# Performance work log

Measured on AMD Instinct MI355X. Metric: run time of the kernel, lower is better.

The kernel has to match this reference:

```python
import jax, jax.numpy as jnp
from jax import lax
import numpy as np


def _qlayer(x, theta):
    """Simulate QLayer: RX(x_i) encoder + trainable RX(theta_i) per wire
    (they commute -> single RX(x_i+theta_i) on |0>), then ring of CNOTs,
    then <Z> on each wire.  x: (B, n) float, theta: (n,). Returns (B, n)."""
    B, n = x.shape
    a = x + theta[None, :]
    c = jnp.cos(a * 0.5)
    s = jnp.sin(a * 0.5)
    # RX(a)|0> = [cos(a/2), -i sin(a/2)] per wire -> product state
    amps = jnp.stack([c + 0j, -1j * s], axis=-1)  # (B, n, 2) complex64
    state = amps[:, 0]  # (B, 2)
    for w in range(1, n):
        state = state[..., None] * amps[:, w].reshape((B,) + (1,) * w + (2,))
    # state: (B, 2, 2, ..., 2), axis w+1 == wire w
    for ctrl in range(n):
        tgt = (ctrl + 1) % n
        s0 = jnp.take(state, 0, axis=ctrl + 1)   # control = 0 block
        s1 = jnp.take(state, 1, axis=ctrl + 1)   # control = 1 block
        t_ax = tgt + 1 if tgt < ctrl else tgt    # target axis after removing ctrl axis
        s1 = jnp.flip(s1, axis=t_ax)             # X on target
        state = jnp.stack([s0, s1], axis=ctrl + 1)
    p = state.real ** 2 + state.imag ** 2
    axes = tuple(range(1, n + 1))
    zs = []
    for w in range(n):
        other = tuple(ax for ax in axes if ax != w + 1)
        pw = jnp.sum(p, axis=other)              # (B, 2)
        zs.append(pw[:, 0] - pw[:, 1])           # <Z_w> = P(0) - P(1)
    return jnp.stack(zs, axis=1)


def setup_inputs() -> dict:
    key = jax.random.key(0)
    ks = jax.random.split(key, 13)
    T, B, D, NQ = 64, 256, 512, 6
    lim = 1.0 / np.sqrt(D + NQ)

    def lin(k):
        k1, k2 = jax.random.split(k)
        W = jax.random.uniform(k1, (D + NQ, NQ), jnp.float32, -lim, lim)
        b = jax.random.uniform(k2, (NQ,), jnp.float32, -lim, lim)
        return W, b

    Wf, bf = lin(ks[0]); Wi, bi = lin(ks[1]); Wu, bu = lin(ks[2]); Wo, bo = lin(ks[3])
    theta_f = jax.random.normal(ks[4], (NQ,), jnp.float32) * 0.1
    theta_i = jax.random.normal(ks[5], (NQ,), jnp.float32) * 0.1
    theta_u = jax.random.normal(ks[6], (NQ,), jnp.float32) * 0.1
    theta_o = jax.random.normal(ks[7], (NQ,), jnp.float32) * 0.1
    inputs = jax.random.normal(ks[8], (T, B, D), jnp.float32)
    return {"inputs": inputs,
            "Wf": Wf, "bf": bf, "Wi": Wi, "bi": bi,
            "Wu": Wu, "bu": bu, "Wo": Wo, "bo": bo,
            "theta_f": theta_f, "theta_i": theta_i,
            "theta_u": theta_u, "theta_o": theta_o}


def reference(inputs, Wf, bf, Wi, bi, Wu, bu, Wo, bo,
              theta_f, theta_i, theta_u, theta_o):
    B = inputs.shape[1]
    NQ = theta_f.shape[0]  # hidden_dim == n_qubits
    h0 = jnp.zeros((B, NQ), inputs.dtype)
    c0 = jnp.zeros((B, NQ), inputs.dtype)

    def step(carry, x):
        hx, cx = carry
        comb = jnp.concatenate([x, hx], axis=1)          # (B, D+NQ)
        f = jax.nn.sigmoid(_qlayer(comb @ Wf + bf, theta_f))
        i = jax.nn.sigmoid(_qlayer(comb @ Wi + bi, theta_i))
        g = jnp.tanh(_qlayer(comb @ Wu + bu, theta_u))
        o = jax.nn.sigmoid(_qlayer(comb @ Wo + bo, theta_o))
        cx2 = f * cx + i * g
        hx2 = o * jnp.tanh(cx2)
        return (hx2, cx2), hx2

    (hx, cx), outputs = lax.scan(step, (h0, c0), inputs)  # outputs: (T, B, NQ)
    return outputs, hx, cx
```

## Files before the change

kernel.cpp:

```cpp
#include <hip/hip_runtime.h>


typedef float v2f __attribute__((ext_vector_type(2)));

__device__ __forceinline__ float fast_rcp(float x) { return __builtin_amdgcn_rcpf(x); }

template <int CTRL>
__device__ __forceinline__ float dpp_add(float x) {
    int t = __builtin_amdgcn_mov_dpp(__float_as_int(x), CTRL, 0xF, 0xF, true);
    return x + __int_as_float(t);
}

template <int G>
__device__ __forceinline__ float quad_bcast(float v) {
    int i = __builtin_amdgcn_mov_dpp(__float_as_int(v), G * 0x55, 0xF, 0xF, true);
    return __int_as_float(i);
}

__global__ __launch_bounds__(512, 2) void gemm_pre(
    const float* __restrict__ X,
    const float* __restrict__ Wf, const float* __restrict__ bf,
    const float* __restrict__ Wi, const float* __restrict__ bi,
    const float* __restrict__ Wu, const float* __restrict__ bu,
    const float* __restrict__ Wo, const float* __restrict__ bo,
    const float* __restrict__ thf, const float* __restrict__ thi,
    const float* __restrict__ thu, const float* __restrict__ tho,
    float* __restrict__ pre)
{
    __shared__ float W_lds[13312];

    const int tid  = threadIdx.x;
    const int w    = tid >> 6;
    const int lane = tid & 63;
    const int rowbase = blockIdx.x * 32;

    #pragma unroll
    for (int i = 0; i < 4; ++i) {
        const float* Wp = (i==0)?Wf:(i==1)?Wi:(i==2)?Wu:Wo;
        int k = tid;
        const float2* s = (const float2*)(Wp + k*6);
        float2* d = (float2*)(W_lds + k*26 + i*6);
        d[0] = s[0]; d[1] = s[1]; d[2] = s[2];
    }
    __syncthreads();

    v2f acc[4][12];
    #pragma unroll
    for (int r = 0; r < 4; ++r)
        #pragma unroll
        for (int p = 0; p < 12; ++p) acc[r][p] = (v2f){0.f, 0.f};

    const float* Xr0 = X + (rowbase + w*4)*512 + lane;

    float pa0 = Xr0[0], pa1 = Xr0[512], pa2 = Xr0[1024], pa3 = Xr0[1536];
    #pragma unroll
    for (int kb = 0; kb < 512; kb += 64) {
        float a0 = pa0, a1 = pa1, a2 = pa2, a3 = pa3;
        if (kb < 448) {
            pa0 = Xr0[kb + 64];
            pa1 = Xr0[kb + 64 + 512];
            pa2 = Xr0[kb + 64 + 1024];
            pa3 = Xr0[kb + 64 + 1536];
        }
        const v2f* wrow = (const v2f*)(W_lds + (kb + lane)*26);
        #pragma unroll
        for (int p = 0; p < 12; ++p) {
            v2f wv = wrow[p];
            acc[0][p] = __builtin_elementwise_fma((v2f){a0,a0}, wv, acc[0][p]);
            acc[1][p] = __builtin_elementwise_fma((v2f){a1,a1}, wv, acc[1][p]);
            acc[2][p] = __builtin_elementwise_fma((v2f){a2,a2}, wv, acc[2][p]);
            acc[3][p] = __builtin_elementwise_fma((v2f){a3,a3}, wv, acc[3][p]);
        }
    }

    #pragma unroll
    for (int r = 0; r < 4; ++r)
        #pragma unroll
        for (int p = 0; p < 12; ++p) {
            float x = acc[r][p].x;
            x = dpp_add<0xB1>(x);
            x = dpp_add<0x4E>(x);
            acc[r][p].x = x;
            float y = acc[r][p].y;
            y = dpp_add<0xB1>(y);
            y = dpp_add<0x4E>(y);
            acc[r][p].y = y;
        }

    #define ACCV(v) ((((v) & 1) == 0) ? acc[(v)/24][((v)%24)/2].x \
                                      : acc[(v)/24][((v)%24)/2].y)
    const int j = lane & 3;
    const int q = lane >> 2;
    const bool j1 = (j & 1) != 0, j2 = (j & 2) != 0;
    float sel[24];
    #pragma unroll
    for (int i = 0; i < 24; ++i) {
        float c0 = ACCV(i*4 + 0), c1 = ACCV(i*4 + 1);
        float c2 = ACCV(i*4 + 2), c3 = ACCV(i*4 + 3);
        float lo = j1 ? c1 : c0;
        float hi = j1 ? c3 : c2;
        sel[i] = j2 ? hi : lo;
    }
    #undef ACCV

    __syncthreads();
    #pragma unroll
    for (int i = 0; i < 24; ++i) {
        W_lds[(w*96 + i*4 + j)*16 + q] = sel[i];
    }
    __syncthreads();

    for (int o = tid; o < 768; o += 512) {
        int ww = o / 96, v = o - ww*96;
        int rr = v / 24, jj24 = v - rr*24;
        const float4* rp = (const float4*)(W_lds + (ww*96 + v)*16);
        float4 r0 = rp[0], r1 = rp[1], r2 = rp[2], r3 = rp[3];
        float s = ((r0.x+r0.y)+(r0.z+r0.w)) + ((r1.x+r1.y)+(r1.z+r1.w))
                + ((r2.x+r2.y)+(r2.z+r2.w)) + ((r3.x+r3.y)+(r3.z+r3.w));
        int g = jj24 / 6, jg = jj24 - g*6;
        const float* bb = (g==0)?bf:(g==1)?bi:(g==2)?bu:bo;
        const float* tt = (g==0)?thf:(g==1)?thi:(g==2)?thu:tho;
        s += bb[jg] + tt[jg];
        int row = rowbase + ww*4 + rr;
        pre[row*24 + jj24] = s;
    }
}

__global__ __launch_bounds__(64, 1) void qlstm_scan(
    const float* __restrict__ pre,
    const float* __restrict__ Wf, const float* __restrict__ Wi,
    const float* __restrict__ Wu, const float* __restrict__ Wo,
    float* __restrict__ out)
{
    const int lane = threadIdx.x;
    const int bl   = lane >> 2;
    const int g    = lane & 3;
    const int b    = blockIdx.x * 16 + bl;

    const float* Wg = (g==0)?Wf:(g==1)?Wi:(g==2)?Wu:Wo;
    float Wh[6][6];
    #pragma unroll
    for (int j = 0; j < 6; ++j)
        #pragma unroll
        for (int w = 0; w < 6; ++w)
            Wh[j][w] = Wg[(512 + j)*6 + w];

    const float k1 = (g==2) ? 2.f : 1.f;
    const float k2 = (g==2) ? 2.f : 1.f;
    const float k3 = (g==2) ? -1.f : 0.f;

    float h[6], c[6];
    #pragma unroll
    for (int w = 0; w < 6; ++w) { h[w] = 0.f; c[w] = 0.f; }

    const float* pb = pre + b*24 + g*6;
    float2 x0 = *(const float2*)(pb);
    float2 x1 = *(const float2*)(pb + 2);
    float2 x2 = *(const float2*)(pb + 4);
    float2 n0 = *(const float2*)(pb + 256*24);
    float2 n1 = *(const float2*)(pb + 256*24 + 2);
    float2 n2 = *(const float2*)(pb + 256*24 + 4);

    for (int t = 0; t < 64; ++t) {
        float xw[6] = {x0.x, x0.y, x1.x, x1.y, x2.x, x2.y};
        x0 = n0; x1 = n1; x2 = n2;
        int tn = (t < 62) ? (t + 2) : 63;
        const float* pn = pre + (tn*256 + b)*24 + g*6;
        n0 = *(const float2*)(pn);
        n1 = *(const float2*)(pn + 2);
        n2 = *(const float2*)(pn + 4);

        float a[6];
        #pragma unroll
        for (int w = 0; w < 6; ++w) {
            float cA = fmaf(h[2], Wh[2][w], fmaf(h[1], Wh[1][w], fmaf(h[0], Wh[0][w], xw[w])));
            float cB = fmaf(h[5], Wh[5][w], fmaf(h[4], Wh[4][w], h[3]*Wh[3][w]));
            a[w] = cA + cB;
        }

        float C[6];
        #pragma unroll
        for (int w = 0; w < 6; ++w) C[w] = __cosf(a[w]);

        float p01 = C[0]*C[1], p23 = C[2]*C[3], p45 = C[4]*C[5];
        float z[6];
        z[1] = p01;
        z[2] = p01*C[2];
        z[3] = p01*p23;
        z[4] = z[3]*C[4];
        z[5] = z[3]*p45;
        z[0] = C[1]*(p23*p45);

        float act[6];
        #pragma unroll
        for (int w = 0; w < 6; ++w) {
            float e = __expf(-k1 * z[w]);
            act[w] = fmaf(k2, fast_rcp(1.f + e), k3);
        }

        float F[6], I[6], U[6], O[6];
        #pragma unroll
        for (int w = 0; w < 6; ++w) {
            F[w] = quad_bcast<0>(act[w]);
            I[w] = quad_bcast<1>(act[w]);
            U[w] = quad_bcast<2>(act[w]);
            O[w] = quad_bcast<3>(act[w]);
        }

        #pragma unroll
        for (int w = 0; w < 6; ++w) {
            c[w] = fmaf(F[w], c[w], I[w]*U[w]);
            float e  = __expf(-2.f * c[w]);
            float tc = fmaf(2.f, fast_rcp(1.f + e), -1.f);
            h[w] = O[w]*tc;
        }

        if (g < 3) {
            float2 v;
            v.x = (g==0) ? h[0] : (g==1) ? h[2] : h[4];
            v.y = (g==0) ? h[1] : (g==1) ? h[3] : h[5];
            *(float2*)(out + (t*256 + b)*6 + g*2) = v;
        }
    }

    if (g < 3) {
        float2 v;
        v.x = (g==0) ? h[0] : (g==1) ? h[2] : h[4];
        v.y = (g==0) ? h[1] : (g==1) ? h[3] : h[5];
        *(float2*)(out + 64*256*6 + b*6 + g*2) = v;
        float2 u;
        u.x = (g==0) ? c[0] : (g==1) ? c[2] : c[4];
        u.y = (g==0) ? c[1] : (g==1) ? c[3] : c[5];
        *(float2*)(out + 64*256*6 + 256*6 + b*6 + g*2) = u;
    }
}

extern "C" void kernel_launch(void* const* d_in, const int* in_sizes, int n_in,
                              void* d_out, int out_size, void* d_ws, size_t ws_size,
                              hipStream_t stream) {
    const float* X   = (const float*)d_in[0];
    const float* Wf  = (const float*)d_in[1];
    const float* bf_ = (const float*)d_in[2];
    const float* Wi  = (const float*)d_in[3];
    const float* bi_ = (const float*)d_in[4];
    const float* Wu  = (const float*)d_in[5];
    const float* bu_ = (const float*)d_in[6];
    const float* Wo  = (const float*)d_in[7];
    const float* bo_ = (const float*)d_in[8];
    const float* thf = (const float*)d_in[9];
    const float* thi = (const float*)d_in[10];
    const float* thu = (const float*)d_in[11];
    const float* tho = (const float*)d_in[12];

    float* pre = (float*)d_ws;
    float* out = (float*)d_out;

    gemm_pre<<<512, 512, 0, stream>>>(X, Wf, bf_, Wi, bi_, Wu, bu_, Wo, bo_,
                                      thf, thi, thu, tho, pre);
    qlstm_scan<<<16, 64, 0, stream>>>(pre, Wf, Wi, Wu, Wo, out);
}
```

Baseline: 141.0 us.

## Double GEMM rows per wave and vectorize scan recurrence with packed FMA

```diff
diff --git a/kernel.cpp b/kernel.cpp
--- a/kernel.cpp
+++ b/kernel.cpp
@@ -32,7 +32,7 @@
     const int tid  = threadIdx.x;
     const int w    = tid >> 6;
     const int lane = tid & 63;
-    const int rowbase = blockIdx.x * 32;
+    const int rowbase = blockIdx.x * 64;
 
     #pragma unroll
     for (int i = 0; i < 4; ++i) {
@@ -44,37 +44,36 @@
     }
     __syncthreads();
 
-    v2f acc[4][12];
-    #pragma unroll
-    for (int r = 0; r < 4; ++r)
+    v2f acc[8][12];
+    #pragma unroll
+    for (int r = 0; r < 8; ++r)
         #pragma unroll
         for (int p = 0; p < 12; ++p) acc[r][p] = (v2f){0.f, 0.f};
 
-    const float* Xr0 = X + (rowbase + w*4)*512 + lane;
-
-    float pa0 = Xr0[0], pa1 = Xr0[512], pa2 = Xr0[1024], pa3 = Xr0[1536];
+    const float* Xr0 = X + (rowbase + w*8)*512 + lane;
+
+    float pa[8];
+    #pragma unroll
+    for (int r = 0; r < 8; ++r) pa[r] = Xr0[r*512];
+
     #pragma unroll
     for (int kb = 0; kb < 512; kb += 64) {
-        float a0 = pa0, a1 = pa1, a2 = pa2, a3 = pa3;
-        if (kb < 448) {
-            pa0 = Xr0[kb + 64];
-            pa1 = Xr0[kb + 64 + 512];
-            pa2 = Xr0[kb + 64 + 1024];
-            pa3 = Xr0[kb + 64 + 1536];
-        }
         const v2f* wrow = (const v2f*)(W_lds + (kb + lane)*26);
         #pragma unroll
         for (int p = 0; p < 12; ++p) {
             v2f wv = wrow[p];
-            acc[0][p] = __builtin_elementwise_fma((v2f){a0,a0}, wv, acc[0][p]);
-            acc[1][p] = __builtin_elementwise_fma((v2f){a1,a1}, wv, acc[1][p]);
-            acc[2][p] = __builtin_elementwise_fma((v2f){a2,a2}, wv, acc[2][p]);
-            acc[3][p] = __builtin_elementwise_fma((v2f){a3,a3}, wv, acc[3][p]);
-        }
-    }
-
-    #pragma unroll
-    for (int r = 0; r < 4; ++r)
+            #pragma unroll
+            for (int r = 0; r < 8; ++r)
+                acc[r][p] = __builtin_elementwise_fma((v2f){pa[r],pa[r]}, wv, acc[r][p]);
+        }
+        if (kb < 448) {
+            #pragma unroll
+            for (int r = 0; r < 8; ++r) pa[r] = Xr0[kb + 64 + r*512];
+        }
+    }
+
+    #pragma unroll
+    for (int r = 0; r < 8; ++r)
         #pragma unroll
         for (int p = 0; p < 12; ++p) {
             float x = acc[r][p].x;
@@ -92,38 +91,41 @@
     const int j = lane & 3;
     const int q = lane >> 2;
     const bool j1 = (j & 1) != 0, j2 = (j & 2) != 0;
-    float sel[24];
-    #pragma unroll
-    for (int i = 0; i < 24; ++i) {
-        float c0 = ACCV(i*4 + 0), c1 = ACCV(i*4 + 1);
-        float c2 = ACCV(i*4 + 2), c3 = ACCV(i*4 + 3);
-        float lo = j1 ? c1 : c0;
-        float hi = j1 ? c3 : c2;
-        sel[i] = j2 ? hi : lo;
+
+    __syncthreads();
+
+    #pragma unroll
+    for (int pass = 0; pass < 2; ++pass) {
+        if ((w >> 2) == pass) {
+            const int w4 = w & 3;
+            #pragma unroll
+            for (int i = 0; i < 48; ++i) {
+                float c0 = ACCV(i*4 + 0), c1 = ACCV(i*4 + 1);
+                float c2 = ACCV(i*4 + 2), c3 = ACCV(i*4 + 3);
+                float lo = j1 ? c1 : c0;
+                float hi = j1 ? c3 : c2;
+                float s  = j2 ? hi : lo;
+                W_lds[(w4*192 + i*4 + j)*16 + q] = s;
+            }
+        }
+        __syncthreads();
+        for (int o = tid; o < 768; o += 512) {
+            int wv4 = o / 192, v = o - wv4*192;
+            int rr = v / 24, col = v - rr*24;
+            const float4* rp = (const float4*)(W_lds + (wv4*192 + v)*16);
+            float4 r0 = rp[0], r1 = rp[1], r2 = rp[2], r3 = rp[3];
+            float s = ((r0.x+r0.y)+(r0.z+r0.w)) + ((r1.x+r1.y)+(r1.z+r1.w))
+                    + ((r2.x+r2.y)+(r2.z+r2.w)) + ((r3.x+r3.y)+(r3.z+r3.w));
+            int g = col / 6, jg = col - g*6;
+            const float* bb = (g==0)?bf:(g==1)?bi:(g==2)?bu:bo;
+            const float* tt = (g==0)?thf:(g==1)?thi:(g==2)?thu:tho;
+            s += bb[jg] + tt[jg];
+            int row = rowbase + (pass*4 + wv4)*8 + rr;
+            pre[row*24 + col] = s;
+        }
+        __syncthreads();
     }
     #undef ACCV
-
-    __syncthreads();
-    #pragma unroll
-    for (int i = 0; i < 24; ++i) {
-        W_lds[(w*96 + i*4 + j)*16 + q] = sel[i];
-    }
-    __syncthreads();
-
-    for (int o = tid; o < 768; o += 512) {
-        int ww = o / 96, v = o - ww*96;
-        int rr = v / 24, jj24 = v - rr*24;
-        const float4* rp = (const float4*)(W_lds + (ww*96 + v)*16);
-        float4 r0 = rp[0], r1 = rp[1], r2 = rp[2], r3 = rp[3];
-        float s = ((r0.x+r0.y)+(r0.z+r0.w)) + ((r1.x+r1.y)+(r1.z+r1.w))
-                + ((r2.x+r2.y)+(r2.z+r2.w)) + ((r3.x+r3.y)+(r3.z+r3.w));
-        int g = jj24 / 6, jg = jj24 - g*6;
-        const float* bb = (g==0)?bf:(g==1)?bi:(g==2)?bu:bo;
-        const float* tt = (g==0)?thf:(g==1)?thi:(g==2)?thu:tho;
-        s += bb[jg] + tt[jg];
-        int row = rowbase + ww*4 + rr;
-        pre[row*24 + jj24] = s;
-    }
 }
 
 __global__ __launch_bounds__(64, 1) void qlstm_scan(
@@ -138,12 +140,12 @@
     const int b    = blockIdx.x * 16 + bl;
 
     const float* Wg = (g==0)?Wf:(g==1)?Wi:(g==2)?Wu:Wo;
-    float Wh[6][6];
+    v2f Wh2[6][3];
     #pragma unroll
     for (int j = 0; j < 6; ++j)
         #pragma unroll
-        for (int w = 0; w < 6; ++w)
-            Wh[j][w] = Wg[(512 + j)*6 + w];
+        for (int p = 0; p < 3; ++p)
+            Wh2[j][p] = (v2f){Wg[(512 + j)*6 + 2*p], Wg[(512 + j)*6 + 2*p + 1]};
 
     const float k1 = (g==2) ? 2.f : 1.f;
     const float k2 = (g==2) ? 2.f : 1.f;
@@ -154,33 +156,34 @@
     for (int w = 0; w < 6; ++w) { h[w] = 0.f; c[w] = 0.f; }
 
     const float* pb = pre + b*24 + g*6;
-    float2 x0 = *(const float2*)(pb);
-    float2 x1 = *(const float2*)(pb + 2);
-    float2 x2 = *(const float2*)(pb + 4);
-    float2 n0 = *(const float2*)(pb + 256*24);
-    float2 n1 = *(const float2*)(pb + 256*24 + 2);
-    float2 n2 = *(const float2*)(pb + 256*24 + 4);
+    v2f x0 = *(const v2f*)(pb);
+    v2f x1 = *(const v2f*)(pb + 2);
+    v2f x2 = *(const v2f*)(pb + 4);
+    v2f n0 = *(const v2f*)(pb + 256*24);
+    v2f n1 = *(const v2f*)(pb + 256*24 + 2);
+    v2f n2 = *(const v2f*)(pb + 256*24 + 4);
 
     for (int t = 0; t < 64; ++t) {
-        float xw[6] = {x0.x, x0.y, x1.x, x1.y, x2.x, x2.y};
+        v2f a2[3] = {x0, x1, x2};
         x0 = n0; x1 = n1; x2 = n2;
         int tn = (t < 62) ? (t + 2) : 63;
         const float* pn = pre + (tn*256 + b)*24 + g*6;
-        n0 = *(const float2*)(pn);
-        n1 = *(const float2*)(pn + 2);
-        n2 = *(const float2*)(pn + 4);
-
-        float a[6];
-        #pragma unroll
-        for (int w = 0; w < 6; ++w) {
-            float cA = fmaf(h[2], Wh[2][w], fmaf(h[1], Wh[1][w], fmaf(h[0], Wh[0][w], xw[w])));
-            float cB = fmaf(h[5], Wh[5][w], fmaf(h[4], Wh[4][w], h[3]*Wh[3][w]));
-            a[w] = cA + cB;
+        n0 = *(const v2f*)(pn);
+        n1 = *(const v2f*)(pn + 2);
+        n2 = *(const v2f*)(pn + 4);
+
+        #pragma unroll
+        for (int j = 0; j < 6; ++j) {
+            v2f hj = (v2f){h[j], h[j]};
+            #pragma unroll
+            for (int p = 0; p < 3; ++p)
+                a2[p] = __builtin_elementwise_fma(hj, Wh2[j][p], a2[p]);
         }
 
         float C[6];
-        #pragma unroll
-        for (int w = 0; w < 6; ++w) C[w] = __cosf(a[w]);
+        C[0] = __cosf(a2[0].x); C[1] = __cosf(a2[0].y);
+        C[2] = __cosf(a2[1].x); C[3] = __cosf(a2[1].y);
+        C[4] = __cosf(a2[2].x); C[5] = __cosf(a2[2].y);
 
         float p01 = C[0]*C[1], p23 = C[2]*C[3], p45 = C[4]*C[5];
         float z[6];
@@ -255,7 +258,7 @@
     float* pre = (float*)d_ws;
     float* out = (float*)d_out;
 
-    gemm_pre<<<512, 512, 0, stream>>>(X, Wf, bf_, Wi, bi_, Wu, bu_, Wo, bo_,
+    gemm_pre<<<256, 512, 0, stream>>>(X, Wf, bf_, Wi, bi_, Wu, bu_, Wo, bo_,
                                       thf, thi, thu, tho, pre);
     qlstm_scan<<<16, 64, 0, stream>>>(pre, Wf, Wi, Wu, Wo, out);
 }
```

Measured after the change: 144.9 us. +2.8%, slower.
